# Kernel optimization log

Hardware: AMD Instinct MI355X
Metric: run time of the kernel (lower is better)

Reference implementation:

```python
import jax, jax.numpy as jnp
import numpy as np

BN_EPS = 1e-5


def conv1x1(x, W, b):
    # x: (B, Cin, H, Wd); W: (Cout, Cin); b: (Cout,)
    return jnp.einsum('bchw,oc->bohw', x, W) + b[None, :, None, None]


def maxpool2x2(x):
    B, C, H, Wd = x.shape
    return x.reshape(B, C, H // 2, 2, Wd // 2, 2).max(axis=(3, 5))


def batchnorm_train(x, gamma, beta):
    # training-mode BN over (B, H, W) per channel, NCHW
    mean = x.mean(axis=(0, 2, 3), keepdims=True)
    var = x.var(axis=(0, 2, 3), keepdims=True)
    xn = (x - mean) * jax.lax.rsqrt(var + BN_EPS)
    return xn * gamma[None, :, None, None] + beta[None, :, None, None]


def setup_inputs() -> dict:
    key = jax.random.key(0)
    ks = jax.random.split(key, 11)
    C, Ci = 256, 128
    scale = 1.0 / np.sqrt(C)
    x = jax.random.normal(ks[0], (4, C, 96, 96), dtype=jnp.float32)
    Wg = jax.random.normal(ks[1], (Ci, C), dtype=jnp.float32) * scale
    bg = jax.random.normal(ks[2], (Ci,), dtype=jnp.float32) * 0.01
    Wt = jax.random.normal(ks[3], (Ci, C), dtype=jnp.float32) * scale
    bt = jax.random.normal(ks[4], (Ci,), dtype=jnp.float32) * 0.01
    Wp = jax.random.normal(ks[5], (Ci, C), dtype=jnp.float32) * scale
    bp = jax.random.normal(ks[6], (Ci,), dtype=jnp.float32) * 0.01
    Ww = jax.random.normal(ks[7], (C, Ci), dtype=jnp.float32) * (1.0 / np.sqrt(Ci))
    bw = jax.random.normal(ks[8], (C,), dtype=jnp.float32) * 0.01
    gamma = jax.random.uniform(ks[9], (C,), dtype=jnp.float32)
    beta = jax.random.normal(ks[10], (C,), dtype=jnp.float32) * 0.01
    return {'x': x, 'Wg': Wg, 'bg': bg, 'Wt': Wt, 'bt': bt, 'Wp': Wp,
            'bp': bp, 'Ww': Ww, 'bw': bw, 'gamma': gamma, 'beta': beta}


def reference(x, Wg, bg, Wt, bt, Wp, bp, Ww, bw, gamma, beta):
    B, C, H, Wd = x.shape
    Ci = Wg.shape[0]
    # g, phi: 1x1 conv then 2x2 maxpool (sub_sample_factor=2)
    g_x = maxpool2x2(conv1x1(x, Wg, bg)).reshape(B, Ci, -1)          # (B, Ci, M)
    phi_x = maxpool2x2(conv1x1(x, Wp, bp)).reshape(B, Ci, -1)        # (B, Ci, M)
    theta_x = conv1x1(x, Wt, bt).reshape(B, Ci, -1)                  # (B, Ci, N)
    # embedded-gaussian attention: softmax(theta^T phi) g^T
    f = jnp.einsum('bcn,bcm->bnm', theta_x, phi_x)                   # (B, N, M)
    a = jax.nn.softmax(f, axis=-1)
    y = jnp.einsum('bnm,bcm->bcn', a, g_x).reshape(B, Ci, H, Wd)
    # W: 1x1 conv + BN (training-mode batch stats), then residual
    W_y = batchnorm_train(conv1x1(y, Ww, bw), gamma, beta)
    return W_y + x
```

## Files before the change

kernel.cpp:

```cpp
#include <hip/hip_runtime.h>
#include <hip/hip_bf16.h>

#define BB 4
#define CC 256
#define CI 128
#define NPIX 9216
#define MPIX 2304
#define WIMG 96
#define WPOOL 48

typedef _Float16 f16x2 __attribute__((ext_vector_type(2)));
typedef _Float16 f16x4 __attribute__((ext_vector_type(4)));
typedef _Float16 f16x8 __attribute__((ext_vector_type(8)));
typedef float f32x4 __attribute__((ext_vector_type(4)));

static __device__ __forceinline__ void gload16(const void* g, void* lds) {
  __builtin_amdgcn_global_load_lds(
      (const __attribute__((address_space(1))) unsigned int*)g,
      (__attribute__((address_space(3))) unsigned int*)lds, 16, 0, 0);
}

__global__ __launch_bounds__(256) void k_prep(
    const float* __restrict__ Wt, const float* __restrict__ Wg,
    const float* __restrict__ Wp, const float* __restrict__ Ww,
    _Float16* __restrict__ Wall, _Float16* __restrict__ Wwh)
{
  int i = blockIdx.x * 256 + threadIdx.x;
  if (i < 98304) {
    int o = i >> 8, c = i & 255;
    float v = (o < 128) ? Wt[o * 256 + c]
            : (o < 256) ? Wg[(o - 128) * 256 + c]
                        : Wp[(o - 256) * 256 + c];
    Wall[i] = (_Float16)v;
  } else {
    int j = i - 98304;
    Wwh[j] = (_Float16)Ww[j];
  }
}

__global__ __launch_bounds__(256) void k_xt(
    const float* __restrict__ x, _Float16* __restrict__ xt)
{
  const int nt = blockIdx.x, ct = blockIdx.y, b = blockIdx.z;
  const int n0 = nt * 64, c0 = ct * 64;
  __shared__ float L[64][65];
  const int t = threadIdx.x;
  #pragma unroll
  for (int i = 0; i < 16; ++i) {
    int idx = i * 256 + t, c = idx >> 6, n = idx & 63;
    L[c][n] = x[(size_t)(b * CC + c0 + c) * NPIX + n0 + n];
  }
  __syncthreads();
  #pragma unroll
  for (int i = 0; i < 4; ++i) {
    int idx = i * 256 + t, n = idx >> 4, cg = idx & 15;
    f16x4 v;
    v[0] = (_Float16)L[cg * 4 + 0][n]; v[1] = (_Float16)L[cg * 4 + 1][n];
    v[2] = (_Float16)L[cg * 4 + 2][n]; v[3] = (_Float16)L[cg * 4 + 3][n];
    *(f16x4*)&xt[(size_t)(b * NPIX + n0 + n) * 256 + c0 + cg * 4] = v;
  }
}

__global__ __launch_bounds__(256) void k_convA(
    const _Float16* __restrict__ xt, const _Float16* __restrict__ Wall,
    const float* __restrict__ bt, const float* __restrict__ bg,
    const float* __restrict__ bp,
    _Float16* __restrict__ th_h, _Float16* __restrict__ gphi)
{
  const int pt = blockIdx.x, ot = blockIdx.y, b = blockIdx.z;
  const int p0 = pt * 128, o0 = ot * 128;
  __shared__ char smem[34816];
  char* WsB = smem;
  char* XsB = smem + 8192;
  const int tid = threadIdx.x;
  const int l = tid & 63, w = tid >> 6;
  const int l15 = l & 15, g16 = l >> 4;
  const int wo = (w & 1) * 64, wp = (w >> 1) * 64;

  f32x4 acc[4][4] = {};
  for (int k0 = 0; k0 < 256; k0 += 32) {
    #pragma unroll
    for (int i = 0; i < 2; ++i) {
      int idx = i * 256 + tid, r = idx >> 2, cg = idx & 3;
      int sw = (cg ^ ((r >> 1) & 3)) * 16;
      *(int4*)(WsB + r * 64 + sw) =
          *(const int4*)&Wall[(size_t)(o0 + r) * 256 + k0 + cg * 8];
      *(int4*)(XsB + r * 64 + sw) =
          *(const int4*)&xt[(size_t)(b * NPIX + p0 + r) * 256 + k0 + cg * 8];
    }
    __syncthreads();
    f16x8 af[4], bf[4];
    #pragma unroll
    for (int f = 0; f < 4; ++f) {
      int ro = wo + f * 16 + l15;
      af[f] = *(const f16x8*)(WsB + ro * 64 + ((g16 ^ ((ro >> 1) & 3)) * 16));
      int rp = wp + f * 16 + l15;
      bf[f] = *(const f16x8*)(XsB + rp * 64 + ((g16 ^ ((rp >> 1) & 3)) * 16));
    }
    #pragma unroll
    for (int of = 0; of < 4; ++of)
      #pragma unroll
      for (int pf = 0; pf < 4; ++pf)
        acc[of][pf] = __builtin_amdgcn_mfma_f32_16x16x32_f16(af[of], bf[pf], acc[of][pf], 0, 0, 0);
    __syncthreads();
  }

  if (o0 == 0) {
    _Float16* T = (_Float16*)smem;
    #pragma unroll
    for (int of = 0; of < 4; ++of) {
      const float4 bb = *(const float4*)&bt[wo + of * 16 + g16 * 4];
      float bv[4] = {bb.x, bb.y, bb.z, bb.w};
      #pragma unroll
      for (int pf = 0; pf < 4; ++pf) {
        f16x4 v;
        #pragma unroll
        for (int r = 0; r < 4; ++r) v[r] = (_Float16)(acc[of][pf][r] + bv[r]);
        *(f16x4*)&T[(wp + pf * 16 + l15) * 136 + wo + of * 16 + g16 * 4] = v;
      }
    }
    __syncthreads();
    #pragma unroll
    for (int i = 0; i < 8; ++i) {
      int idx = i * 256 + tid, row = idx >> 4, cg = idx & 15;
      *(int4*)&th_h[(size_t)(b * NPIX + p0 + row) * 128 + cg * 8] =
          *(const int4*)&T[row * 136 + cg * 8];
    }
  } else {
    const float* bsel = (o0 == 128) ? bg : bp;
    const int chbase = o0 - 128;
    #pragma unroll
    for (int of = 0; of < 4; ++of) {
      const float4 bb = *(const float4*)&bsel[wo + of * 16 + g16 * 4];
      float bv[4] = {bb.x, bb.y, bb.z, bb.w};
      #pragma unroll
      for (int pf = 0; pf < 4; ++pf)
        #pragma unroll
        for (int r = 0; r < 4; ++r) {
          int ch = chbase + wo + of * 16 + g16 * 4 + r;
          gphi[(size_t)(b * 256 + ch) * NPIX + p0 + wp + pf * 16 + l15] =
              (_Float16)(acc[of][pf][r] + bv[r]);
        }
    }
  }
}

__global__ __launch_bounds__(256) void k_pool2(
    const _Float16* __restrict__ gphi,
    _Float16* __restrict__ g_h, _Float16* __restrict__ phi_h)
{
  const int mt = blockIdx.x, ct = blockIdx.y, b = blockIdx.z;
  const int m0 = mt * 64, c0 = ct * 32;
  __shared__ _Float16 Lg[32][72], Lp[32][72];
  const int t = threadIdx.x;
  #pragma unroll
  for (int i = 0; i < 8; ++i) {
    int idx = i * 256 + t, c = idx >> 6, m = idx & 63;
    int mm = m0 + m, hp = mm / WPOOL, wp = mm % WPOOL;
    const _Float16* sg = &gphi[(size_t)(b * 256 + c0 + c) * NPIX + hp * 192 + wp * 2];
    f16x2 a0 = *(const f16x2*)sg;
    f16x2 a1 = *(const f16x2*)(sg + WIMG);
    Lg[c][m] = (_Float16)fmaxf(fmaxf((float)a0[0], (float)a0[1]),
                               fmaxf((float)a1[0], (float)a1[1]));
    const _Float16* sp = sg + (size_t)128 * NPIX;
    f16x2 b0 = *(const f16x2*)sp;
    f16x2 b1 = *(const f16x2*)(sp + WIMG);
    Lp[c][m] = (_Float16)fmaxf(fmaxf((float)b0[0], (float)b0[1]),
                               fmaxf((float)b1[0], (float)b1[1]));
  }
  __syncthreads();
  {
    int c = t >> 3, mq = t & 7;
    f16x8 v = *(const f16x8*)&Lg[c][mq * 8];
    *(f16x8*)&g_h[(size_t)(b * CI + c0 + c) * MPIX + m0 + mq * 8] = v;
  }
  #pragma unroll
  for (int i = 0; i < 2; ++i) {
    int idx = i * 256 + t, m = idx >> 3, cg = idx & 7;
    f16x4 v;
    v[0] = Lp[cg * 4 + 0][m]; v[1] = Lp[cg * 4 + 1][m];
    v[2] = Lp[cg * 4 + 2][m]; v[3] = Lp[cg * 4 + 3][m];
    *(f16x4*)&phi_h[(size_t)(b * MPIX + m0 + m) * 128 + c0 + cg * 4] = v;
  }
}

__global__ __launch_bounds__(256, 2) void k_attn(
    const _Float16* __restrict__ th_h,
    const _Float16* __restrict__ phi_h,
    const _Float16* __restrict__ g_h,
    _Float16* __restrict__ y_part,
    float2* __restrict__ ml)
{
  const int qt = blockIdx.x, b = blockIdx.y, split = blockIdx.z;
  const int n0 = qt * 128;
  const int kt0 = split * 18;
  __shared__ char smem[65536];
  char* const PlB = smem + 49152;

  const int tid = threadIdx.x;
  const int l = tid & 63, wid = tid >> 6;
  const int l15 = l & 15, g16 = l >> 4;
  const int wq0 = wid * 32;

  f16x8 thf[2][4];
  #pragma unroll
  for (int qh = 0; qh < 2; ++qh) {
    const size_t row = (size_t)(b * NPIX + n0 + wq0 + 16 * qh + l15) * 128;
    #pragma unroll
    for (int cs = 0; cs < 4; ++cs)
      thf[qh][cs] = *(const f16x8*)&th_h[row + 32 * cs + 8 * g16];
  }

  auto stage_phi = [&](int bufsel, int kt) {
    char* dst = smem + bufsel * 16384;
    const int m1 = kt * 64;
    #pragma unroll
    for (int j = 0; j < 4; ++j) {
      int mbase = wid * 16 + j * 4;
      int m = mbase + (l >> 4);
      int cg = (l & 15) ^ (m & 7);
      gload16(&phi_h[((size_t)(b * MPIX + m1 + m) << 7) + cg * 8],
              dst + mbase * 256);
    }
  };
  auto stage_g = [&](int kt) {
    char* dst = smem + 32768;
    const int m1 = kt * 64;
    #pragma unroll
    for (int j = 0; j < 4; ++j) {
      int cbase = wid * 32 + j * 8;
      int c = cbase + (l >> 3);
      int cg = (l & 7) ^ (c & 7);
      gload16(&g_h[(size_t)(b * CI + c) * MPIX + m1 + cg * 8],
              dst + cbase * 128);
    }
  };

  stage_phi(0, kt0);
  __syncthreads();

  f32x4 yacc[2][8] = {};
  float mrun[2] = {-1e30f, -1e30f};
  float lrun[2] = {0.f, 0.f};

  #pragma unroll 1
  for (int kt = kt0; kt < kt0 + 18; ++kt) {
    stage_g(kt);
    const char* phC = smem + ((kt - kt0) & 1) * 16384;

    f32x4 sacc[4][2] = {};
    #pragma unroll
    for (int cs = 0; cs < 4; ++cs) {
      const int cb = cs * 64 + g16 * 16;
      #pragma unroll
      for (int mf = 0; mf < 4; ++mf) {
        const int m = 16 * mf + l15;
        f16x8 aph = *(const f16x8*)(phC + m * 256 + (cb ^ ((m & 7) << 4)));
        sacc[mf][0] = __builtin_amdgcn_mfma_f32_16x16x32_f16(aph, thf[0][cs], sacc[mf][0], 0, 0, 0);
        sacc[mf][1] = __builtin_amdgcn_mfma_f32_16x16x32_f16(aph, thf[1][cs], sacc[mf][1], 0, 0, 0);
      }
    }

    float scl2[2];
    f16x4 pr[4][2];
    #pragma unroll
    for (int qh = 0; qh < 2; ++qh) {
      float mx = -1e30f;
      #pragma unroll
      for (int mf = 0; mf < 4; ++mf)
        #pragma unroll
        for (int r = 0; r < 4; ++r) mx = fmaxf(mx, sacc[mf][qh][r]);
      mx = fmaxf(mx, __shfl_xor(mx, 16, 64));
      mx = fmaxf(mx, __shfl_xor(mx, 32, 64));
      const float mo = mrun[qh];
      const float mn = fmaxf(mo, mx);
      float sum = 0.f;
      #pragma unroll
      for (int mf = 0; mf < 4; ++mf)
        #pragma unroll
        for (int r = 0; r < 4; ++r) {
          float p = __expf(sacc[mf][qh][r] - mn);
          _Float16 ph = (_Float16)p;
          pr[mf][qh][r] = ph;
          sum += (float)ph;
        }
      sum += __shfl_xor(sum, 16, 64);
      sum += __shfl_xor(sum, 32, 64);
      const float sc = __expf(mo - mn);
      scl2[qh] = sc;
      lrun[qh] = lrun[qh] * sc + sum;
      mrun[qh] = mn;
    }

    #pragma unroll
    for (int qh = 0; qh < 2; ++qh) {
      const int qw = l15 + 16 * qh;
      char* prow = PlB + (wid << 12) + qw * 128;
      #pragma unroll
      for (int mf = 0; mf < 4; ++mf)
        *(f16x4*)(prow + ((32 * mf + 8 * g16) ^ ((qw & 7) << 4))) = pr[mf][qh];
    }

    {
      float rs[2][4];
      #pragma unroll
      for (int r = 0; r < 4; ++r) {
        rs[0][r] = __shfl(scl2[0], 4 * g16 + r, 64);
        rs[1][r] = __shfl(scl2[1], 4 * g16 + r, 64);
      }
      #pragma unroll
      for (int qi = 0; qi < 2; ++qi)
        #pragma unroll
        for (int cf = 0; cf < 8; ++cf)
          #pragma unroll
          for (int r = 0; r < 4; ++r)
            yacc[qi][cf][r] *= rs[qi][r];
    }

    __syncthreads();

    if (kt + 1 < kt0 + 18)
      stage_phi((kt + 1 - kt0) & 1, kt + 1);

    #pragma unroll
    for (int ms = 0; ms < 2; ++ms) {
      const int mb = ms * 64 + g16 * 16;
      const int q0w = l15, q1w = l15 + 16;
      f16x8 pa0 = *(const f16x8*)(PlB + (wid << 12) + q0w * 128 + (mb ^ ((q0w & 7) << 4)));
      f16x8 pa1 = *(const f16x8*)(PlB + (wid << 12) + q1w * 128 + (mb ^ ((q1w & 7) << 4)));
      #pragma unroll
      for (int cf = 0; cf < 8; ++cf) {
        const int c = 16 * cf + l15;
        f16x8 gb = *(const f16x8*)(smem + 32768 + c * 128 + (mb ^ ((c & 7) << 4)));
        yacc[0][cf] = __builtin_amdgcn_mfma_f32_16x16x32_f16(pa0, gb, yacc[0][cf], 0, 0, 0);
        yacc[1][cf] = __builtin_amdgcn_mfma_f32_16x16x32_f16(pa1, gb, yacc[1][cf], 0, 0, 0);
      }
    }

    __syncthreads();
  }

  if (g16 == 0) {
    #pragma unroll
    for (int qh = 0; qh < 2; ++qh)
      ml[(size_t)(split * BB + b) * NPIX + n0 + wq0 + 16 * qh + l15] =
          make_float2(mrun[qh], lrun[qh]);
  }
  _Float16* Yl = (_Float16*)smem;
  #pragma unroll
  for (int qi = 0; qi < 2; ++qi)
    #pragma unroll
    for (int cf = 0; cf < 8; ++cf)
      #pragma unroll
      for (int r = 0; r < 4; ++r)
        Yl[(wq0 + 16 * qi + 4 * g16 + r) * 136 + 16 * cf + l15] =
            (_Float16)yacc[qi][cf][r];
  __syncthreads();
  #pragma unroll
  for (int i = 0; i < 8; ++i) {
    int idx = i * 256 + tid, row = idx >> 4, cg = idx & 15;
    *(int4*)&y_part[(size_t)((split * BB + b) * NPIX + n0 + row) * 128 + cg * 8] =
        *(const int4*)&Yl[row * 136 + cg * 8];
  }
}

__global__ __launch_bounds__(256) void k_comb(
    const _Float16* __restrict__ y_part, const float2* __restrict__ ml,
    _Float16* __restrict__ y_h)
{
  int idx = blockIdx.x * 256 + threadIdx.x;
  int cg = idx & 15;
  int n  = (idx >> 4) % NPIX;
  int b  = (idx >> 4) / NPIX;
  float2 a0 = ml[(size_t)b * NPIX + n];
  float2 a1 = ml[(size_t)(BB + b) * NPIX + n];
  float M = fmaxf(a0.x, a1.x);
  float w0 = __expf(a0.x - M), w1 = __expf(a1.x - M);
  float inv = 1.0f / (w0 * a0.y + w1 * a1.y);
  w0 *= inv; w1 *= inv;
  f16x8 v0 = *(const f16x8*)&y_part[(size_t)(b * NPIX + n) * 128 + cg * 8];
  f16x8 v1 = *(const f16x8*)&y_part[(size_t)((BB + b) * NPIX + n) * 128 + cg * 8];
  f16x8 o;
  #pragma unroll
  for (int r = 0; r < 8; ++r)
    o[r] = (_Float16)(w0 * (float)v0[r] + w1 * (float)v1[r]);
  *(f16x8*)&y_h[(size_t)(b * NPIX + n) * 128 + cg * 8] = o;
}

__global__ __launch_bounds__(256) void k_wconv(
    const _Float16* __restrict__ y_h, const _Float16* __restrict__ Wwh,
    const float* __restrict__ bw, float* __restrict__ zbuf)
{
  const int nt = blockIdx.x, ot = blockIdx.y, b = blockIdx.z;
  const int n0 = nt * 128, o0 = ot * 128;
  __shared__ char smem[16384];
  char* WsB = smem;
  char* YsB = smem + 8192;
  const int tid = threadIdx.x;
  const int l = tid & 63, w = tid >> 6;
  const int l15 = l & 15, g16 = l >> 4;
  const int wo = (w & 1) * 64, wn = (w >> 1) * 64;

  f32x4 acc[4][4] = {};
  for (int k0 = 0; k0 < 128; k0 += 32) {
    #pragma unroll
    for (int i = 0; i < 2; ++i) {
      int idx = i * 256 + tid, r = idx >> 2, cg = idx & 3;
      int sw = (cg ^ ((r >> 1) & 3)) * 16;
      *(int4*)(WsB + r * 64 + sw) =
          *(const int4*)&Wwh[(size_t)(o0 + r) * 128 + k0 + cg * 8];
      *(int4*)(YsB + r * 64 + sw) =
          *(const int4*)&y_h[(size_t)(b * NPIX + n0 + r) * 128 + k0 + cg * 8];
    }
    __syncthreads();
    f16x8 af[4], bf[4];
    #pragma unroll
    for (int f = 0; f < 4; ++f) {
      int ro = wo + f * 16 + l15;
      af[f] = *(const f16x8*)(WsB + ro * 64 + ((g16 ^ ((ro >> 1) & 3)) * 16));
      int rn = wn + f * 16 + l15;
      bf[f] = *(const f16x8*)(YsB + rn * 64 + ((g16 ^ ((rn >> 1) & 3)) * 16));
    }
    #pragma unroll
    for (int of = 0; of < 4; ++of)
      #pragma unroll
      for (int pf = 0; pf < 4; ++pf)
        acc[of][pf] = __builtin_amdgcn_mfma_f32_16x16x32_f16(af[of], bf[pf], acc[of][pf], 0, 0, 0);
    __syncthreads();
  }
  #pragma unroll
  for (int of = 0; of < 4; ++of) {
    const float4 bb = *(const float4*)&bw[o0 + wo + of * 16 + g16 * 4];
    float bv[4] = {bb.x, bb.y, bb.z, bb.w};
    #pragma unroll
    for (int pf = 0; pf < 4; ++pf)
      #pragma unroll
      for (int r = 0; r < 4; ++r)
        zbuf[(size_t)(b * CC + o0 + wo + of * 16 + g16 * 4 + r) * NPIX +
             n0 + wn + pf * 16 + l15] = acc[of][pf][r] + bv[r];
  }
}

__global__ __launch_bounds__(256) void k_stats(
    const float* __restrict__ zbuf, float* __restrict__ stats)
{
  const int o = blockIdx.x, t = threadIdx.x;
  float s = 0.f, s2 = 0.f;
  for (int b = 0; b < BB; ++b) {
    const float* z = &zbuf[(size_t)(b * CC + o) * NPIX];
    for (int i = t; i < NPIX / 4; i += 256) {
      float4 v = *(const float4*)&z[i * 4];
      s  += v.x + v.y + v.z + v.w;
      s2 += v.x * v.x + v.y * v.y + v.z * v.z + v.w * v.w;
    }
  }
  #pragma unroll
  for (int off = 1; off < 64; off <<= 1) {
    s  += __shfl_xor(s,  off, 64);
    s2 += __shfl_xor(s2, off, 64);
  }
  __shared__ float ls[4], ls2[4];
  if ((t & 63) == 0) { ls[t >> 6] = s; ls2[t >> 6] = s2; }
  __syncthreads();
  if (t == 0) {
    float S  = ls[0] + ls[1] + ls[2] + ls[3];
    float S2 = ls2[0] + ls2[1] + ls2[2] + ls2[3];
    const float invn = 1.0f / (float)(BB * NPIX);
    float mean = S * invn;
    float var  = S2 * invn - mean * mean;
    stats[o] = mean;
    stats[CC + o] = rsqrtf(var + 1e-5f);
  }
}

__global__ __launch_bounds__(256) void k_out(
    const float* __restrict__ zbuf, const float* __restrict__ x,
    const float* __restrict__ gamma, const float* __restrict__ beta,
    const float* __restrict__ stats, float* __restrict__ out)
{
  int idx = blockIdx.x * 256 + threadIdx.x;
  const int total4 = BB * CC * NPIX / 4;
  if (idx >= total4) return;
  size_t e = (size_t)idx * 4;
  int p = (int)(e % NPIX);
  int o = (int)((e / NPIX) % CC);
  int b = (int)(e / ((size_t)CC * NPIX));
  float a  = stats[CC + o] * gamma[o];
  float c0 = beta[o] - stats[o] * a;
  float4 z  = *(const float4*)&zbuf[(size_t)(b * CC + o) * NPIX + p];
  float4 xv = *(const float4*)&x[e];
  float4 rv;
  rv.x = z.x * a + c0 + xv.x;
  rv.y = z.y * a + c0 + xv.y;
  rv.z = z.z * a + c0 + xv.z;
  rv.w = z.w * a + c0 + xv.w;
  *(float4*)&out[e] = rv;
}

extern "C" void kernel_launch(void* const* d_in, const int* in_sizes, int n_in,
                              void* d_out, int out_size, void* d_ws, size_t ws_size,
                              hipStream_t stream)
{
  const float* x     = (const float*)d_in[0];
  const float* Wg    = (const float*)d_in[1];
  const float* bg    = (const float*)d_in[2];
  const float* Wt    = (const float*)d_in[3];
  const float* bt    = (const float*)d_in[4];
  const float* Wp    = (const float*)d_in[5];
  const float* bp    = (const float*)d_in[6];
  const float* Ww    = (const float*)d_in[7];
  const float* bw    = (const float*)d_in[8];
  const float* gamma = (const float*)d_in[9];
  const float* beta  = (const float*)d_in[10];
  float* out = (float*)d_out;

  char* wsb = (char*)d_ws;
  float*    zbuf   = (float*)wsb;
  _Float16* xt     = (_Float16*)wsb;
  _Float16* y_part = (_Float16*)wsb;
  char* p2 = wsb + 37748736;
  _Float16* gphi  = (_Float16*)p2;
  _Float16* y_h   = (_Float16*)p2;
  char* p3 = p2 + 18874368;
  _Float16* th_h  = (_Float16*)p3;
  _Float16* g_h   = (_Float16*)(p3 + 9437184);
  _Float16* phi_h = (_Float16*)(p3 + 11796480);
  _Float16* Wall  = (_Float16*)(p3 + 14155776);
  _Float16* Wwh   = (_Float16*)(p3 + 14352384);
  float*    stats = (float*)(p3 + 14417920);
  float2*   ml    = (float2*)(p3 + 14420992);

  k_prep<<<512, 256, 0, stream>>>(Wt, Wg, Wp, Ww, Wall, Wwh);

  dim3 gxt(NPIX / 64, CC / 64, BB);
  k_xt<<<gxt, 256, 0, stream>>>(x, xt);

  dim3 g1(NPIX / 128, 3, BB);
  k_convA<<<g1, 256, 0, stream>>>(xt, Wall, bt, bg, bp, th_h, gphi);

  dim3 g2(MPIX / 64, 4, BB);
  k_pool2<<<g2, 256, 0, stream>>>(gphi, g_h, phi_h);

  dim3 g3(NPIX / 128, BB, 2);
  k_attn<<<g3, 256, 0, stream>>>(th_h, phi_h, g_h, y_part, ml);

  k_comb<<<(BB * NPIX * 16) / 256, 256, 0, stream>>>(y_part, ml, y_h);

  dim3 g4(NPIX / 128, CC / 128, BB);
  k_wconv<<<g4, 256, 0, stream>>>(y_h, Wwh, bw, zbuf);

  k_stats<<<CC, 256, 0, stream>>>(zbuf, stats);

  k_out<<<(BB * CC * NPIX / 4 + 255) / 256, 256, 0, stream>>>(zbuf, x, gamma, beta, stats, out);
}
```

Baseline: 174.7 us.

## Use exp2 with prescaled theta, lazy softmax rescale, single-buffer phi LDS

Theta is prescaled by log2(e) when it is written out, so the attention and combine kernels can use exp2f instead of __expf. The online-softmax rescale of the output accumulators now runs only when some row max in the wavefront grows by more than 8 (base 2). Otherwise the stale max is kept, which lets fp16 probabilities reach up to 256. The phi tile is single-buffered, cutting attention LDS from 64KB to 48KB, which could allow more resident blocks. The cost is less overlap of the phi load with compute and a small precision risk from the larger unnormalised probabilities.

After: 184.4 us. 5.6% more time.

```diff
diff --git a/kernel.cpp b/kernel.cpp
--- a/kernel.cpp
+++ b/kernel.cpp
@@ -8,6 +8,7 @@
 #define MPIX 2304
 #define WIMG 96
 #define WPOOL 48
+#define LOG2E 1.4426950408889634f
 
 typedef _Float16 f16x2 __attribute__((ext_vector_type(2)));
 typedef _Float16 f16x4 __attribute__((ext_vector_type(4)));
@@ -115,7 +116,8 @@
       for (int pf = 0; pf < 4; ++pf) {
         f16x4 v;
         #pragma unroll
-        for (int r = 0; r < 4; ++r) v[r] = (_Float16)(acc[of][pf][r] + bv[r]);
+        for (int r = 0; r < 4; ++r)
+          v[r] = (_Float16)((acc[of][pf][r] + bv[r]) * LOG2E);
         *(f16x4*)&T[(wp + pf * 16 + l15) * 136 + wo + of * 16 + g16 * 4] = v;
       }
     }
@@ -194,8 +196,9 @@
   const int qt = blockIdx.x, b = blockIdx.y, split = blockIdx.z;
   const int n0 = qt * 128;
   const int kt0 = split * 18;
-  __shared__ char smem[65536];
-  char* const PlB = smem + 49152;
+  __shared__ char smem[49152];
+  char* const GlB = smem + 16384;
+  char* const PlB = smem + 32768;
 
   const int tid = threadIdx.x;
   const int l = tid & 63, wid = tid >> 6;
@@ -211,8 +214,7 @@
       thf[qh][cs] = *(const f16x8*)&th_h[row + 32 * cs + 8 * g16];
   }
 
-  auto stage_phi = [&](int bufsel, int kt) {
-    char* dst = smem + bufsel * 16384;
+  auto stage_phi = [&](int kt) {
     const int m1 = kt * 64;
     #pragma unroll
     for (int j = 0; j < 4; ++j) {
@@ -220,11 +222,10 @@
       int m = mbase + (l >> 4);
       int cg = (l & 15) ^ (m & 7);
       gload16(&phi_h[((size_t)(b * MPIX + m1 + m) << 7) + cg * 8],
-              dst + mbase * 256);
+              smem + mbase * 256);
     }
   };
   auto stage_g = [&](int kt) {
-    char* dst = smem + 32768;
     const int m1 = kt * 64;
     #pragma unroll
     for (int j = 0; j < 4; ++j) {
@@ -232,11 +233,11 @@
       int c = cbase + (l >> 3);
       int cg = (l & 7) ^ (c & 7);
       gload16(&g_h[(size_t)(b * CI + c) * MPIX + m1 + cg * 8],
-              dst + cbase * 128);
+              GlB + cbase * 128);
     }
   };
 
-  stage_phi(0, kt0);
+  stage_phi(kt0);
   __syncthreads();
 
   f32x4 yacc[2][8] = {};
@@ -246,7 +247,6 @@
   #pragma unroll 1
   for (int kt = kt0; kt < kt0 + 18; ++kt) {
     stage_g(kt);
-    const char* phC = smem + ((kt - kt0) & 1) * 16384;
 
     f32x4 sacc[4][2] = {};
     #pragma unroll
@@ -255,41 +255,65 @@
       #pragma unroll
       for (int mf = 0; mf < 4; ++mf) {
         const int m = 16 * mf + l15;
-        f16x8 aph = *(const f16x8*)(phC + m * 256 + (cb ^ ((m & 7) << 4)));
+        f16x8 aph = *(const f16x8*)(smem + m * 256 + (cb ^ ((m & 7) << 4)));
         sacc[mf][0] = __builtin_amdgcn_mfma_f32_16x16x32_f16(aph, thf[0][cs], sacc[mf][0], 0, 0, 0);
         sacc[mf][1] = __builtin_amdgcn_mfma_f32_16x16x32_f16(aph, thf[1][cs], sacc[mf][1], 0, 0, 0);
       }
     }
 
-    float scl2[2];
-    f16x4 pr[4][2];
+    float mx[2];
     #pragma unroll
     for (int qh = 0; qh < 2; ++qh) {
-      float mx = -1e30f;
+      float m0 = -1e30f;
       #pragma unroll
       for (int mf = 0; mf < 4; ++mf)
         #pragma unroll
-        for (int r = 0; r < 4; ++r) mx = fmaxf(mx, sacc[mf][qh][r]);
-      mx = fmaxf(mx, __shfl_xor(mx, 16, 64));
-      mx = fmaxf(mx, __shfl_xor(mx, 32, 64));
-      const float mo = mrun[qh];
-      const float mn = fmaxf(mo, mx);
+        for (int r = 0; r < 4; ++r) m0 = fmaxf(m0, sacc[mf][qh][r]);
+      m0 = fmaxf(m0, __shfl_xor(m0, 16, 64));
+      m0 = fmaxf(m0, __shfl_xor(m0, 32, 64));
+      mx[qh] = m0;
+    }
+    const int nskip = !__all((mx[0] <= mrun[0] + 8.f) & (mx[1] <= mrun[1] + 8.f));
+    if (nskip) {
+      float scl2[2];
+      #pragma unroll
+      for (int qh = 0; qh < 2; ++qh) {
+        const float mn = fmaxf(mrun[qh], mx[qh]);
+        scl2[qh] = exp2f(mrun[qh] - mn);
+        lrun[qh] *= scl2[qh];
+        mrun[qh] = mn;
+      }
+      float rs[2][4];
+      #pragma unroll
+      for (int r = 0; r < 4; ++r) {
+        rs[0][r] = __shfl(scl2[0], 4 * g16 + r, 64);
+        rs[1][r] = __shfl(scl2[1], 4 * g16 + r, 64);
+      }
+      #pragma unroll
+      for (int qi = 0; qi < 2; ++qi)
+        #pragma unroll
+        for (int cf = 0; cf < 8; ++cf)
+          #pragma unroll
+          for (int r = 0; r < 4; ++r)
+            yacc[qi][cf][r] *= rs[qi][r];
+    }
+
+    f16x4 pr[4][2];
+    #pragma unroll
+    for (int qh = 0; qh < 2; ++qh) {
       float sum = 0.f;
       #pragma unroll
       for (int mf = 0; mf < 4; ++mf)
         #pragma unroll
         for (int r = 0; r < 4; ++r) {
-          float p = __expf(sacc[mf][qh][r] - mn);
+          float p = exp2f(sacc[mf][qh][r] - mrun[qh]);
           _Float16 ph = (_Float16)p;
           pr[mf][qh][r] = ph;
           sum += (float)ph;
         }
       sum += __shfl_xor(sum, 16, 64);
       sum += __shfl_xor(sum, 32, 64);
-      const float sc = __expf(mo - mn);
-      scl2[qh] = sc;
-      lrun[qh] = lrun[qh] * sc + sum;
-      mrun[qh] = mn;
+      lrun[qh] += sum;
     }
 
     #pragma unroll
@@ -301,26 +325,10 @@
         *(f16x4*)(prow + ((32 * mf + 8 * g16) ^ ((qw & 7) << 4))) = pr[mf][qh];
     }
 
-    {
-      float rs[2][4];
-      #pragma unroll
-      for (int r = 0; r < 4; ++r) {
-        rs[0][r] = __shfl(scl2[0], 4 * g16 + r, 64);
-        rs[1][r] = __shfl(scl2[1], 4 * g16 + r, 64);
-      }
-      #pragma unroll
-      for (int qi = 0; qi < 2; ++qi)
-        #pragma unroll
-        for (int cf = 0; cf < 8; ++cf)
-          #pragma unroll
-          for (int r = 0; r < 4; ++r)
-            yacc[qi][cf][r] *= rs[qi][r];
-    }
-
     __syncthreads();
 
     if (kt + 1 < kt0 + 18)
-      stage_phi((kt + 1 - kt0) & 1, kt + 1);
+      stage_phi(kt + 1);
 
     #pragma unroll
     for (int ms = 0; ms < 2; ++ms) {
@@ -331,7 +339,7 @@
       #pragma unroll
       for (int cf = 0; cf < 8; ++cf) {
         const int c = 16 * cf + l15;
-        f16x8 gb = *(const f16x8*)(smem + 32768 + c * 128 + (mb ^ ((c & 7) << 4)));
+        f16x8 gb = *(const f16x8*)(GlB + c * 128 + (mb ^ ((c & 7) << 4)));
         yacc[0][cf] = __builtin_amdgcn_mfma_f32_16x16x32_f16(pa0, gb, yacc[0][cf], 0, 0, 0);
         yacc[1][cf] = __builtin_amdgcn_mfma_f32_16x16x32_f16(pa1, gb, yacc[1][cf], 0, 0, 0);
       }
@@ -375,7 +383,7 @@
   float2 a0 = ml[(size_t)b * NPIX + n];
   float2 a1 = ml[(size_t)(BB + b) * NPIX + n];
   float M = fmaxf(a0.x, a1.x);
-  float w0 = __expf(a0.x - M), w1 = __expf(a1.x - M);
+  float w0 = exp2f(a0.x - M), w1 = exp2f(a1.x - M);
   float inv = 1.0f / (w0 * a0.y + w1 * a1.y);
   w0 *= inv; w1 *= inv;
   f16x8 v0 = *(const f16x8*)&y_part[(size_t)(b * NPIX + n) * 128 + cg * 8];
```
